# Kernel tuning notes

Hardware: AMD Instinct MI355X
Metric: run time of the kernel (lower is better)

## Reference

```python
import jax, jax.numpy as jnp
import numpy as np

B, T = 512, 200
N_SKILLS, M, DK, DV, H = 1000, 50, 64, 64, 128


def setup_inputs() -> dict:
    key = jax.random.key(0)
    ks = jax.random.split(key, 12)
    inp = {
        'skill_seq': jax.random.randint(ks[0], (B, T), 0, N_SKILLS, dtype=jnp.int32),
        'correct_seq': jax.random.randint(ks[1], (B, T), 0, 2, dtype=jnp.int32),
        'mask': jnp.ones((B, T), dtype=jnp.float32),
        'skill_embed': jax.random.normal(ks[2], (N_SKILLS, DK), dtype=jnp.float32),
        'key_memory': jax.random.normal(ks[3], (M, DK), dtype=jnp.float32) * 0.1,
        'value_init': jnp.zeros((M, DV), dtype=jnp.float32),
        'interaction_embed': jax.random.normal(ks[4], (2 * N_SKILLS, DV), dtype=jnp.float32),
        'erase_W': jax.random.normal(ks[5], (DV, DV), dtype=jnp.float32) * 0.05,
        'erase_b': jnp.zeros((DV,), dtype=jnp.float32),
        'add_W': jax.random.normal(ks[6], (DV, DV), dtype=jnp.float32) * 0.05,
        'add_b': jnp.zeros((DV,), dtype=jnp.float32),
        'fc1_W': jax.random.normal(ks[7], (DK + DV, H), dtype=jnp.float32) * 0.05,
        'fc1_b': jnp.zeros((H,), dtype=jnp.float32),
        'fc2_W': jax.random.normal(ks[8], (H, 1), dtype=jnp.float32) * 0.05,
        'fc2_b': jnp.zeros((1,), dtype=jnp.float32),
    }
    return inp


def reference(skill_seq, correct_seq, mask, skill_embed, key_memory, value_init,
              interaction_embed, erase_W, erase_b, add_W, add_b,
              fc1_W, fc1_b, fc2_W, fc2_b):
    n_skills = skill_embed.shape[0]
    b = skill_seq.shape[0]
    # Time-invariant-per-step quantities are precomputed vectorized over (B,T):
    q = skill_embed[skill_seq]                                   # (B,T,dk)
    w = jax.nn.softmax(jnp.einsum('btk,mk->btm', q, key_memory), axis=-1)  # (B,T,M)
    v = interaction_embed[skill_seq + correct_seq * n_skills]    # (B,T,dv)
    e = jax.nn.sigmoid(v @ erase_W + erase_b)                    # (B,T,dv)
    a = jnp.tanh(v @ add_W + add_b)                              # (B,T,dv)

    def step(mem, inputs):
        # mem: (B,M,dv); read BEFORE write, matching the torch loop
        w_t, e_t, a_t = inputs                                   # (B,M),(B,dv),(B,dv)
        read = jnp.einsum('bm,bmv->bv', w_t, mem)                # (B,dv)
        we = w_t[:, :, None]                                     # (B,M,1)
        mem = mem * (1.0 - we * e_t[:, None, :]) + we * a_t[:, None, :]
        return mem, read

    mem0 = jnp.broadcast_to(value_init, (b,) + value_init.shape)
    _, reads = jax.lax.scan(step, mem0,
                            (jnp.swapaxes(w, 0, 1), jnp.swapaxes(e, 0, 1), jnp.swapaxes(a, 0, 1)))
    reads = jnp.swapaxes(reads, 0, 1)                            # (B,T,dv)

    x = jnp.concatenate([q, reads], axis=-1)                     # (B,T,dk+dv)
    h = jax.nn.relu(x @ fc1_W + fc1_b)
    logit = (h @ fc2_W + fc2_b)[..., 0]
    p = jax.nn.sigmoid(logit)
    return p * mask, correct_seq.astype(jnp.float32) * mask
```

## Files before the change

kernel.cpp:

```cpp
#include <hip/hip_runtime.h>
#include <hip/hip_bf16.h>

#define B_  512
#define T_  200
#define NS  1000
#define M_  50
#define DK  64
#define DV  64
#define H_  128
#define NPOS (B_ * T_)

typedef __hip_bfloat16 bf16;
typedef unsigned short ushort_t;
typedef __bf16 bf16x8 __attribute__((ext_vector_type(8)));
typedef float  f32x4  __attribute__((ext_vector_type(4)));

__device__ __forceinline__ float ldf(const void* p, int i, int isbf) {
    return isbf ? __bfloat162float(((const bf16*)p)[i]) : ((const float*)p)[i];
}
__device__ __forceinline__ int sniff(const void* mask) {
    return (*(const unsigned*)mask == 0x3F800000u) ? 0 : 1;
}
__device__ __forceinline__ float rl(float x, int l) {
    return __int_as_float(__builtin_amdgcn_readlane(__float_as_int(x), l));
}
__device__ __forceinline__ ushort_t f2bf(float v) {
    bf16 h = __float2bfloat16(v);
    return *(ushort_t*)&h;
}

__global__ __launch_bounds__(256) void dk31_tabs(
    const int*  __restrict__ cseq,
    const void* __restrict__ mask,
    const void* __restrict__ skill_embed, const void* __restrict__ key_memory,
    const void* __restrict__ inter,
    const void* __restrict__ eW, const void* __restrict__ eb,
    const void* __restrict__ aW, const void* __restrict__ ab,
    const void* __restrict__ fc1W, const void* __restrict__ fc1b,
    float* __restrict__ w_tab, unsigned* __restrict__ ea_tab,
    float* __restrict__ hq2, ushort_t* __restrict__ W2f,
    float* __restrict__ out1) {
    int isbf = sniff(mask);
    int lane = threadIdx.x & 63;
    int gwid = (blockIdx.x << 2) | (threadIdx.x >> 6);

    if (gwid < NS) {
        int s = gwid;
        float q = ldf(skill_embed, s * DK + lane, isbf);
        float acc = 0.f;
        if (lane < M_) {
            #pragma unroll 16
            for (int k = 0; k < DK; ++k)
                acc = fmaf(rl(q, k), ldf(key_memory, lane * DK + k, isbf), acc);
        }
        float val = (lane < M_) ? acc : -1e30f;
        float mx = val;
        #pragma unroll
        for (int off = 1; off < 64; off <<= 1) mx = fmaxf(mx, __shfl_xor(mx, off, 64));
        float ex = (lane < M_) ? __expf(val - mx) : 0.f;
        float sm = ex;
        #pragma unroll
        for (int off = 1; off < 64; off <<= 1) sm += __shfl_xor(sm, off, 64);
        w_tab[s * 64 + lane] = (lane < M_) ? ex / sm : 0.f;
    } else if (gwid < 3 * NS) {
        int r = gwid - NS;
        float vv = ldf(inter, r * DV + lane, isbf);
        float eacc = ldf(eb, lane, isbf);
        float aacc = ldf(ab, lane, isbf);
        #pragma unroll 16
        for (int u = 0; u < DV; ++u) {
            float vu = rl(vv, u);
            eacc = fmaf(vu, ldf(eW, u * DV + lane, isbf), eacc);
            aacc = fmaf(vu, ldf(aW, u * DV + lane, isbf), aacc);
        }
        float ev = 1.f / (1.f + __expf(-eacc));
        float av = tanhf(aacc);
        ea_tab[r * 64 + lane] = ((unsigned)f2bf(av) << 16) | (unsigned)f2bf(ev);
    } else if (gwid < 4 * NS) {
        int s = gwid - 3 * NS;
        float q = ldf(skill_embed, s * DK + lane, isbf);
        float acc0 = ldf(fc1b, lane, isbf);
        float acc1 = ldf(fc1b, 64 + lane, isbf);
        #pragma unroll 16
        for (int k = 0; k < DK; ++k) {
            float qk = rl(q, k);
            acc0 = fmaf(qk, ldf(fc1W, k * H_ + lane, isbf), acc0);
            acc1 = fmaf(qk, ldf(fc1W, k * H_ + 64 + lane, isbf), acc1);
        }
        hq2[s * H_ + (lane & 15) * 8 +     (lane >> 4)] = acc0;
        hq2[s * H_ + (lane & 15) * 8 + 4 + (lane >> 4)] = acc1;
    } else if (gwid < 4 * NS + 16) {
        int f = gwid - 4 * NS;
        int tile = f >> 1, kk = f & 1;
        int n = tile * 16 + (lane & 15);
        #pragma unroll
        for (int j = 0; j < 8; ++j) {
            int v = kk * 32 + (lane >> 4) * 8 + j;
            W2f[(f * 64 + lane) * 8 + j] = f2bf(ldf(fc1W, (DK + v) * H_ + n, isbf));
        }
    } else if (gwid < 4 * NS + 16 + 400) {
        int qp = gwid - (4 * NS + 16);
        int t0 = qp * 256;
        #pragma unroll
        for (int i = 0; i < 4; ++i) {
            int idx = t0 + i * 64 + lane;
            out1[idx] = (float)cseq[idx] * ldf(mask, idx, isbf);
        }
    }
}


#define FSCROW(W, MEM) \
    acc0 = fmaf(W.x, MEM.x, acc0); \
    acc1 = fmaf(W.y, MEM.y, acc1); \
    acc2 = fmaf(W.z, MEM.z, acc2); \
    acc3 = fmaf(W.w, MEM.w, acc3); \
    MEM.x = fmaf(-W.x, fmaf(e0, MEM.x, -a0), MEM.x); \
    MEM.y = fmaf(-W.y, fmaf(e0, MEM.y, -a0), MEM.y); \
    MEM.z = fmaf(-W.z, fmaf(e0, MEM.z, -a0), MEM.z); \
    MEM.w = fmaf(-W.w, fmaf(e0, MEM.w, -a0), MEM.w);

#define FSTEP(EAR, WARR, TP, TT) { \
    float e0 = __uint_as_float(EAR << 16); \
    float a0 = __uint_as_float(EAR & 0xFFFF0000u); \
    float acc0 = 0.f, acc1 = 0.f, acc2 = 0.f, acc3 = 0.f; \
    FSCROW(WARR[0], mem[0]) FSCROW(WARR[1], mem[1]) \
    FSCROW(WARR[2], mem[2]) FSCROW(WARR[3], mem[3]) \
    rbf[buf * 4096 + (TP) * 256 + (((k << 6) | lane) ^ (((TP) & 7) << 3))] = \
        f2bf((acc0 + acc1) + (acc2 + acc3)); \
    EAR = ea_tab[(s2 + c2 * NS) * 64 + lane]; \
    WARR[0] = w4[s2 * 16 + 4 * k + 0]; \
    WARR[1] = w4[s2 * 16 + 4 * k + 1]; \
    WARR[2] = w4[s2 * 16 + 4 * k + 2]; \
    WARR[3] = w4[s2 * 16 + 4 * k + 3]; \
    s2 = s3; c2 = c3; \
    { int tf = (TT) + 4; tf = tf < T_ ? tf : T_ - 1; \
      s3 = ss[base + tf]; c3 = cs[base + tf]; } }

__global__ __launch_bounds__(256, 2) void dk31_fused(
    const int*  __restrict__ ss, const int* __restrict__ cs,
    const void* __restrict__ mask, const void* __restrict__ value_init,
    const float* __restrict__ w_tab, const unsigned* __restrict__ ea_tab,
    const float* __restrict__ hq2, const ushort_t* __restrict__ W2f,
    const void* __restrict__ fc2W, const void* __restrict__ fc2b,
    float* __restrict__ out0) {

    __shared__ ushort_t rb[2][16][256];
    __shared__ float    xs[4][16];

    int isbf = sniff(mask);
    int lane = threadIdx.x & 63;
    int k    = threadIdx.x >> 6;
    int b    = blockIdx.x;
    const int base = b * T_;
    const float4* w4 = (const float4*)w_tab;
    int col = lane & 15, quad = lane >> 4;
    ushort_t* rbf = &rb[0][0][0];

    const bf16x8* B8 = (const bf16x8*)W2f;
    bf16x8 bA0 = B8[(2 * (2 * k)    ) * 64 + lane];
    bf16x8 bA1 = B8[(2 * (2 * k) + 1) * 64 + lane];
    bf16x8 bB0 = B8[(2 * (2 * k + 1)    ) * 64 + lane];
    bf16x8 bB1 = B8[(2 * (2 * k + 1) + 1) * 64 + lane];
    float f2wA = ldf(fc2W, (2 * k)     * 16 + col, isbf);
    float f2wB = ldf(fc2W, (2 * k + 1) * 16 + col, isbf);
    float f2b  = ldf(fc2b, 0, isbf);

    float4 mem[4];
    #pragma unroll
    for (int i = 0; i < 4; ++i) {
        int r = 16 * k + 4 * i;
        mem[i].x = (r + 0 < M_) ? ldf(value_init, (r + 0) * DV + lane, isbf) : 0.f;
        mem[i].y = (r + 1 < M_) ? ldf(value_init, (r + 1) * DV + lane, isbf) : 0.f;
        mem[i].z = (r + 2 < M_) ? ldf(value_init, (r + 2) * DV + lane, isbf) : 0.f;
        mem[i].w = (r + 3 < M_) ? ldf(value_init, (r + 3) * DV + lane, isbf) : 0.f;
    }

    int s2 = ss[base + 2], c2 = cs[base + 2];
    int s3 = ss[base + 3], c3 = cs[base + 3];

    float4 wa[4], wb[4];
    unsigned eaA, eaB;
    {
        int sA = ss[base], cA = cs[base];
        eaA = ea_tab[(sA + cA * NS) * 64 + lane];
        #pragma unroll
        for (int i = 0; i < 4; ++i) wa[i] = w4[sA * 16 + 4 * k + i];
        int sB = ss[base + 1], cB = cs[base + 1];
        eaB = ea_tab[(sB + cB * NS) * 64 + lane];
        #pragma unroll
        for (int i = 0; i < 4; ++i) wb[i] = w4[sB * 16 + 4 * k + i];
    }

    for (int cc = 0; cc < 13; ++cc) {
        int buf   = cc & 1;
        int p0    = cc * 16;
        int nstep = (cc == 12) ? 8 : 16;

        for (int tp = 0; tp < nstep; tp += 2) {
            int t = p0 + tp;
            FSTEP(eaA, wa, tp,     t)
            FSTEP(eaB, wb, tp + 1, t + 1)
        }
        __syncthreads();

        {
            int pA = p0 + quad * 4;
            int i0 = pA + 0 < T_ ? pA + 0 : T_ - 1;
            int i1 = pA + 1 < T_ ? pA + 1 : T_ - 1;
            int i2 = pA + 2 < T_ ? pA + 2 : T_ - 1;
            int i3 = pA + 3 < T_ ? pA + 3 : T_ - 1;
            int sp0 = ss[base + i0], sp1 = ss[base + i1];
            int sp2 = ss[base + i2], sp3 = ss[base + i3];
            float2 h0 = *(const float2*)(hq2 + sp0 * H_ + col * 8 + 2 * k);
            float2 h1 = *(const float2*)(hq2 + sp1 * H_ + col * 8 + 2 * k);
            float2 h2 = *(const float2*)(hq2 + sp2 * H_ + col * 8 + 2 * k);
            float2 h3 = *(const float2*)(hq2 + sp3 * H_ + col * 8 + 2 * k);

            f32x4 cA = {0.f, 0.f, 0.f, 0.f}, cB = {0.f, 0.f, 0.f, 0.f};
            const bf16x8* A8 = (const bf16x8*)&rb[buf][0][0];
            #pragma unroll
            for (int kk = 0; kk < 8; ++kk) {
                bf16x8 av = A8[(col * 32 + kk * 4 + quad) ^ (col & 7)];
                if (kk & 1) {
                    cA = __builtin_amdgcn_mfma_f32_16x16x32_bf16(av, bA1, cA, 0, 0, 0);
                    cB = __builtin_amdgcn_mfma_f32_16x16x32_bf16(av, bB1, cB, 0, 0, 0);
                } else {
                    cA = __builtin_amdgcn_mfma_f32_16x16x32_bf16(av, bA0, cA, 0, 0, 0);
                    cB = __builtin_amdgcn_mfma_f32_16x16x32_bf16(av, bB0, cB, 0, 0, 0);
                }
            }
            float x0, x1, x2, x3, h;
            h = cA.x + h0.x; x0  = fmaxf(h, 0.f) * f2wA;
            h = cB.x + h0.y; x0 += fmaxf(h, 0.f) * f2wB;
            h = cA.y + h1.x; x1  = fmaxf(h, 0.f) * f2wA;
            h = cB.y + h1.y; x1 += fmaxf(h, 0.f) * f2wB;
            h = cA.z + h2.x; x2  = fmaxf(h, 0.f) * f2wA;
            h = cB.z + h2.y; x2 += fmaxf(h, 0.f) * f2wB;
            h = cA.w + h3.x; x3  = fmaxf(h, 0.f) * f2wA;
            h = cB.w + h3.y; x3 += fmaxf(h, 0.f) * f2wB;
            #pragma unroll
            for (int off = 1; off < 16; off <<= 1) {
                x0 += __shfl_xor(x0, off, 64);
                x1 += __shfl_xor(x1, off, 64);
                x2 += __shfl_xor(x2, off, 64);
                x3 += __shfl_xor(x3, off, 64);
            }
            if (col == 0) {
                xs[k][quad * 4 + 0] = x0;
                xs[k][quad * 4 + 1] = x1;
                xs[k][quad * 4 + 2] = x2;
                xs[k][quad * 4 + 3] = x3;
            }
        }
        __syncthreads();

        if (k == 0 && lane < 16 && p0 + lane < T_) {
            int p = base + p0 + lane;
            float xsum = xs[0][lane] + xs[1][lane] + xs[2][lane] + xs[3][lane] + f2b;
            float mk = ldf(mask, p, isbf);
            out0[p] = mk / (1.f + __expf(-xsum));
        }
    }
}

extern "C" void kernel_launch(void* const* d_in, const int* in_sizes, int n_in,
                              void* d_out, int out_size, void* d_ws, size_t ws_size,
                              hipStream_t stream) {
    const int*  skill_seq   = (const int*)d_in[0];
    const int*  correct_seq = (const int*)d_in[1];
    const void* mask        = d_in[2];
    const void* skill_embed = d_in[3];
    const void* key_memory  = d_in[4];
    const void* value_init  = d_in[5];
    const void* inter       = d_in[6];
    const void* erase_W     = d_in[7];
    const void* erase_b     = d_in[8];
    const void* add_W       = d_in[9];
    const void* add_b       = d_in[10];
    const void* fc1_W       = d_in[11];
    const void* fc1_b       = d_in[12];
    const void* fc2_W       = d_in[13];
    const void* fc2_b       = d_in[14];
    float* out = (float*)d_out;

    float*    ws      = (float*)d_ws + 16;
    float*    w_tab   = ws;
    unsigned* ea_tab  = (unsigned*)(ws + 64000);
    float*    hq2     = ws + 192000;
    ushort_t* W2f     = (ushort_t*)(ws + 320000);

    dk31_tabs<<<1104, 256, 0, stream>>>(correct_seq, mask, skill_embed, key_memory,
                                        inter, erase_W, erase_b, add_W, add_b,
                                        fc1_W, fc1_b,
                                        w_tab, ea_tab, hq2, W2f,
                                        out + (size_t)NPOS);

    dk31_fused<<<B_, 256, 0, stream>>>(skill_seq, correct_seq, mask, value_init,
                                       w_tab, ea_tab, hq2, W2f, fc2_W, fc2_b,
                                       out);
}
```

Measured before the change: 167.7 us.

## Double-buffer output partials, drop a barrier, and prefetch hq2 during the scan

Double-buffers the xs partial-sum array so each chunk's output sigmoid is written after the next chunk's barrier, which removes one __syncthreads per chunk. The step loop is fully unrolled, and the skill index and hq2 gathers for the MLP epilogue are issued between recurrence steps so their latency overlaps the scan. The aim is to take barrier and load latency off the serial recurrence critical path. The cost is more live registers under launch_bounds(256,2), plus a separate tail write for the last chunk after the loop.

New measurement: 160.8 us. 4.1% less time.

```diff
diff --git a/kernel.cpp b/kernel.cpp
--- a/kernel.cpp
+++ b/kernel.cpp
@@ -29,7 +29,7 @@
     return *(ushort_t*)&h;
 }
 
-__global__ __launch_bounds__(256) void dk31_tabs(
+__global__ __launch_bounds__(256) void dk32_tabs(
     const int*  __restrict__ cseq,
     const void* __restrict__ mask,
     const void* __restrict__ skill_embed, const void* __restrict__ key_memory,
@@ -137,7 +137,7 @@
     { int tf = (TT) + 4; tf = tf < T_ ? tf : T_ - 1; \
       s3 = ss[base + tf]; c3 = cs[base + tf]; } }
 
-__global__ __launch_bounds__(256, 2) void dk31_fused(
+__global__ __launch_bounds__(256, 2) void dk32_fused(
     const int*  __restrict__ ss, const int* __restrict__ cs,
     const void* __restrict__ mask, const void* __restrict__ value_init,
     const float* __restrict__ w_tab, const unsigned* __restrict__ ea_tab,
@@ -146,7 +146,7 @@
     float* __restrict__ out0) {
 
     __shared__ ushort_t rb[2][16][256];
-    __shared__ float    xs[4][16];
+    __shared__ float    xs[2][4][16];
 
     int isbf = sniff(mask);
     int lane = threadIdx.x & 63;
@@ -195,28 +195,42 @@
     for (int cc = 0; cc < 13; ++cc) {
         int buf   = cc & 1;
         int p0    = cc * 16;
-        int nstep = (cc == 12) ? 8 : 16;
-
-        for (int tp = 0; tp < nstep; tp += 2) {
-            int t = p0 + tp;
-            FSTEP(eaA, wa, tp,     t)
-            FSTEP(eaB, wb, tp + 1, t + 1)
+
+        FSTEP(eaA, wa, 0, p0 + 0) FSTEP(eaB, wb, 1, p0 + 1)
+
+        int pA = p0 + quad * 4;
+        int i0 = pA + 0 < T_ ? pA + 0 : T_ - 1;
+        int i1 = pA + 1 < T_ ? pA + 1 : T_ - 1;
+        int i2 = pA + 2 < T_ ? pA + 2 : T_ - 1;
+        int i3 = pA + 3 < T_ ? pA + 3 : T_ - 1;
+        int sp0 = ss[base + i0], sp1 = ss[base + i1];
+        int sp2 = ss[base + i2], sp3 = ss[base + i3];
+
+        FSTEP(eaA, wa, 2, p0 + 2) FSTEP(eaB, wb, 3, p0 + 3)
+
+        float2 h0 = *(const float2*)(hq2 + sp0 * H_ + col * 8 + 2 * k);
+        float2 h1 = *(const float2*)(hq2 + sp1 * H_ + col * 8 + 2 * k);
+        float2 h2 = *(const float2*)(hq2 + sp2 * H_ + col * 8 + 2 * k);
+        float2 h3 = *(const float2*)(hq2 + sp3 * H_ + col * 8 + 2 * k);
+
+        FSTEP(eaA, wa, 4, p0 + 4) FSTEP(eaB, wb, 5, p0 + 5)
+        FSTEP(eaA, wa, 6, p0 + 6) FSTEP(eaB, wb, 7, p0 + 7)
+        if (cc != 12) {
+            FSTEP(eaA, wa,  8, p0 +  8) FSTEP(eaB, wb,  9, p0 +  9)
+            FSTEP(eaA, wa, 10, p0 + 10) FSTEP(eaB, wb, 11, p0 + 11)
+            FSTEP(eaA, wa, 12, p0 + 12) FSTEP(eaB, wb, 13, p0 + 13)
+            FSTEP(eaA, wa, 14, p0 + 14) FSTEP(eaB, wb, 15, p0 + 15)
         }
         __syncthreads();
 
+        if (cc > 0 && k == 0 && lane < 16) {
+            int p = base + (cc - 1) * 16 + lane;
+            float xsum = xs[buf ^ 1][0][lane] + xs[buf ^ 1][1][lane]
+                       + xs[buf ^ 1][2][lane] + xs[buf ^ 1][3][lane] + f2b;
+            out0[p] = ldf(mask, p, isbf) / (1.f + __expf(-xsum));
+        }
+
         {
-            int pA = p0 + quad * 4;
-            int i0 = pA + 0 < T_ ? pA + 0 : T_ - 1;
-            int i1 = pA + 1 < T_ ? pA + 1 : T_ - 1;
-            int i2 = pA + 2 < T_ ? pA + 2 : T_ - 1;
-            int i3 = pA + 3 < T_ ? pA + 3 : T_ - 1;
-            int sp0 = ss[base + i0], sp1 = ss[base + i1];
-            int sp2 = ss[base + i2], sp3 = ss[base + i3];
-            float2 h0 = *(const float2*)(hq2 + sp0 * H_ + col * 8 + 2 * k);
-            float2 h1 = *(const float2*)(hq2 + sp1 * H_ + col * 8 + 2 * k);
-            float2 h2 = *(const float2*)(hq2 + sp2 * H_ + col * 8 + 2 * k);
-            float2 h3 = *(const float2*)(hq2 + sp3 * H_ + col * 8 + 2 * k);
-
             f32x4 cA = {0.f, 0.f, 0.f, 0.f}, cB = {0.f, 0.f, 0.f, 0.f};
             const bf16x8* A8 = (const bf16x8*)&rb[buf][0][0];
             #pragma unroll
@@ -247,20 +261,20 @@
                 x3 += __shfl_xor(x3, off, 64);
             }
             if (col == 0) {
-                xs[k][quad * 4 + 0] = x0;
-                xs[k][quad * 4 + 1] = x1;
-                xs[k][quad * 4 + 2] = x2;
-                xs[k][quad * 4 + 3] = x3;
+                xs[buf][k][quad * 4 + 0] = x0;
+                xs[buf][k][quad * 4 + 1] = x1;
+                xs[buf][k][quad * 4 + 2] = x2;
+                xs[buf][k][quad * 4 + 3] = x3;
             }
         }
-        __syncthreads();
-
-        if (k == 0 && lane < 16 && p0 + lane < T_) {
-            int p = base + p0 + lane;
-            float xsum = xs[0][lane] + xs[1][lane] + xs[2][lane] + xs[3][lane] + f2b;
-            float mk = ldf(mask, p, isbf);
-            out0[p] = mk / (1.f + __expf(-xsum));
-        }
+    }
+
+    __syncthreads();
+    if (k == 0 && lane < 16 && 192 + lane < T_) {
+        int p = base + 192 + lane;
+        float xsum = xs[0][0][lane] + xs[0][1][lane]
+                   + xs[0][2][lane] + xs[0][3][lane] + f2b;
+        out0[p] = ldf(mask, p, isbf) / (1.f + __expf(-xsum));
     }
 }
 
@@ -290,13 +304,13 @@
     float*    hq2     = ws + 192000;
     ushort_t* W2f     = (ushort_t*)(ws + 320000);
 
-    dk31_tabs<<<1104, 256, 0, stream>>>(correct_seq, mask, skill_embed, key_memory,
+    dk32_tabs<<<1104, 256, 0, stream>>>(correct_seq, mask, skill_embed, key_memory,
                                         inter, erase_W, erase_b, add_W, add_b,
                                         fc1_W, fc1_b,
                                         w_tab, ea_tab, hq2, W2f,
                                         out + (size_t)NPOS);
 
-    dk31_fused<<<B_, 256, 0, stream>>>(skill_seq, correct_seq, mask, value_init,
+    dk32_fused<<<B_, 256, 0, stream>>>(skill_seq, correct_seq, mask, value_init,
                                        w_tab, ea_tab, hq2, W2f, fc2_W, fc2_b,
                                        out);
 }
```
